# Optimization experiments

Hardware: AMD Instinct MI355X
Metric: run time of the kernel (lower is better)

## Reference

```python
import jax, jax.numpy as jnp
import numpy as np

MAX_DISP = 4  # init kwarg


def setup_inputs() -> dict:
    key = jax.random.key(0)
    k1, k2 = jax.random.split(key)
    x_1 = jax.random.normal(k1, (8, 128, 128, 128), dtype=jnp.float32)
    x_2 = jax.random.normal(k2, (8, 128, 128, 128), dtype=jnp.float32)
    return {"x_1": x_1, "x_2": x_2}


def reference(x_1, x_2):
    d = MAX_DISP
    H, W = x_1.shape[2], x_1.shape[3]
    # zero-pad x_2 by max_disp on both spatial dims (ConstantPad2d)
    x2p = jnp.pad(x_2, ((0, 0), (0, 0), (d, d), (d, d)))
    # loop over the fixed (2d+1)^2 = 81 displacement offsets (structural, not data dim)
    outs = [
        jnp.mean(x_1 * x2p[:, :, dx:dx + H, dy:dy + W], axis=1)  # [B,H,W]
        for dx in range(2 * d + 1)
        for dy in range(2 * d + 1)
    ]
    return jnp.stack(outs, axis=1)  # [B, 81, H, W]
```

## Files before the change

### kernel.cpp

```cpp
#include <hip/hip_runtime.h>


constexpr int Bn = 8, Cn = 128, Hn = 128, Wn = 128;
constexpr int HWn = Hn * Wn;
constexpr int TH = 4;
constexpr int NDH = 3;
constexpr int NR = TH + NDH - 1;
constexpr int WP = 144;
constexpr int NF4 = (NR * 140) / 4;

__global__ __launch_bounds__(256, 3)
void corr_kernel(const float* __restrict__ x1, const float* __restrict__ x2,
                 float* __restrict__ out) {
  __shared__ float s2[2][2][NR][WP];
  __shared__ float sred[128][36];

  const int t    = threadIdx.x;
  const int half = t >> 7;
  const int q    = t & 127;
  const int row  = q >> 5;
  const int w0   = (q & 31) << 2;

  const int phys = blockIdx.x;
  const int xcd  = phys & 7;
  const int slot = phys >> 3;
  const int tl   = slot / 3;
  const int g    = slot % 3;
  const int tile = xcd * 32 + tl;
  const int b    = tile >> 5;
  const int h0   = (tile & 31) * TH;
  const int dhm  = g * NDH - 4;

  const int i0 = q, i1 = q + 128;
  const int sr0 = i0 / 35, fc0 = i0 % 35;
  int sr1 = i1 / 35; const int fc1 = i1 % 35;
  const bool act1 = (i1 < NF4);
  if (sr1 > NR - 1) sr1 = NR - 1;
  const int gr0 = h0 + dhm + sr0;
  const int gr1 = h0 + dhm + sr1;
  const bool ok0 = ((unsigned)gr0 < (unsigned)Hn) && (fc0 >= 1) && (fc0 <= 32);
  const bool ok1 = act1 && ((unsigned)gr1 < (unsigned)Hn) && (fc1 >= 1) && (fc1 <= 32);
  const int off0 = gr0 * Wn + fc0 * 4 - 4;
  const int off1 = gr1 * Wn + fc1 * 4 - 4;

  const float* x1c = x1 + (size_t)b * Cn * HWn + (size_t)(half * 64) * HWn
                        + (h0 + row) * Wn + w0;
  const float* x2c = x2 + (size_t)b * Cn * HWn + (size_t)(half * 64) * HWn;

  float4 acc[NDH][9];
#pragma unroll
  for (int r = 0; r < NDH; ++r)
#pragma unroll
    for (int dw = 0; dw < 9; ++dw) acc[r][dw] = make_float4(0.f, 0.f, 0.f, 0.f);

  float4 pv0 = make_float4(0.f, 0.f, 0.f, 0.f);
  float4 pv1 = make_float4(0.f, 0.f, 0.f, 0.f);
  if (ok0) pv0 = *(const float4*)(x2c + off0);
  if (ok1) pv1 = *(const float4*)(x2c + off1);
  float4 pa = *(const float4*)x1c;

#pragma unroll 1
  for (int cc = 0; cc < 64; ++cc) {
    const int buf = cc & 1;
    *(float4*)&s2[buf][half][sr0][fc0 * 4] = pv0;
    if (act1) *(float4*)&s2[buf][half][sr1][fc1 * 4] = pv1;
    const float4 a = pa;
    if (cc < 63) {
      const float* nx2 = x2c + (size_t)(cc + 1) * HWn;
      if (ok0) pv0 = *(const float4*)(nx2 + off0);
      if (ok1) pv1 = *(const float4*)(nx2 + off1);
      pa = *(const float4*)(x1c + (size_t)(cc + 1) * HWn);
    }
    __syncthreads();

#pragma unroll
    for (int r = 0; r < NDH; ++r) {
      const float* srow = &s2[buf][half][row + r][w0];
      const float4 wa = *(const float4*)(srow);
      const float4 wb = *(const float4*)(srow + 4);
      const float4 wc = *(const float4*)(srow + 8);
      const float win[12] = {wa.x, wa.y, wa.z, wa.w, wb.x, wb.y, wb.z, wb.w,
                             wc.x, wc.y, wc.z, wc.w};
#pragma unroll
      for (int dw = 0; dw < 9; ++dw) {
        acc[r][dw].x += a.x * win[dw + 0];
        acc[r][dw].y += a.y * win[dw + 1];
        acc[r][dw].z += a.z * win[dw + 2];
        acc[r][dw].w += a.w * win[dw + 3];
      }
    }
  }

  const float scale = 1.0f / 128.0f;
  float* ob = out + (size_t)b * 81 * HWn + (size_t)(h0 + row) * Wn + w0;
#pragma unroll
  for (int r = 0; r < NDH; ++r) {
    if (half) {
#pragma unroll
      for (int dw = 0; dw < 9; ++dw) *(float4*)&sred[q][dw * 4] = acc[r][dw];
    }
    __syncthreads();
    if (!half) {
      const int obase = (g * 3 + r) * 9;
#pragma unroll
      for (int dw = 0; dw < 9; ++dw) {
        const float4 s = *(const float4*)&sred[q][dw * 4];
        const float4 m = acc[r][dw];
        float4 rz;
        rz.x = (m.x + s.x) * scale;
        rz.y = (m.y + s.y) * scale;
        rz.z = (m.z + s.z) * scale;
        rz.w = (m.w + s.w) * scale;
        *(float4*)(ob + (size_t)(obase + dw) * HWn) = rz;
      }
    }
    __syncthreads();
  }
}

extern "C" void kernel_launch(void* const* d_in, const int* in_sizes, int n_in,
                              void* d_out, int out_size, void* d_ws, size_t ws_size,
                              hipStream_t stream) {
  const float* x1 = (const float*)d_in[0];
  const float* x2 = (const float*)d_in[1];
  float* out = (float*)d_out;
  const int n_wgs = Bn * (Hn / TH) * 3;
  corr_kernel<<<dim3(n_wgs), dim3(256), 0, stream>>>(x1, x2, out);
}
```

Measured before the change: 189.1 us.

## Give each wavefront a private LDS window to drop per-channel block barriers

Splits the shared x2 staging buffer so each of the four wavefronts stages its own 4-row window for the two output rows it computes. Because each wave only reads data it wrote itself, the per-channel __syncthreads and the double buffering are removed. It relies on in-order LDS access within a single wave. The cost is some duplicated global loads of the overlapping halo rows across the two waves of each channel half, plus a third load per lane.

```diff
diff --git a/kernel.cpp b/kernel.cpp
--- a/kernel.cpp
+++ b/kernel.cpp
@@ -5,21 +5,23 @@
 constexpr int HWn = Hn * Wn;
 constexpr int TH = 4;
 constexpr int NDH = 3;
-constexpr int NR = TH + NDH - 1;
+constexpr int WR = 4;
 constexpr int WP = 144;
-constexpr int NF4 = (NR * 140) / 4;
 
 __global__ __launch_bounds__(256, 3)
 void corr_kernel(const float* __restrict__ x1, const float* __restrict__ x2,
                  float* __restrict__ out) {
-  __shared__ float s2[2][2][NR][WP];
+  __shared__ float s2[4][WR][WP];
   __shared__ float sred[128][36];
 
   const int t    = threadIdx.x;
-  const int half = t >> 7;
+  const int wv   = t >> 6;
+  const int lane = t & 63;
+  const int half = wv >> 1;
+  const int rp   = wv & 1;
   const int q    = t & 127;
-  const int row  = q >> 5;
-  const int w0   = (q & 31) << 2;
+  const int rowl = q >> 5;
+  const int w0   = (lane & 31) << 2;
 
   const int phys = blockIdx.x;
   const int xcd  = phys & 7;
@@ -31,21 +33,24 @@
   const int h0   = (tile & 31) * TH;
   const int dhm  = g * NDH - 4;
 
-  const int i0 = q, i1 = q + 128;
-  const int sr0 = i0 / 35, fc0 = i0 % 35;
-  int sr1 = i1 / 35; const int fc1 = i1 % 35;
-  const bool act1 = (i1 < NF4);
-  if (sr1 > NR - 1) sr1 = NR - 1;
-  const int gr0 = h0 + dhm + sr0;
-  const int gr1 = h0 + dhm + sr1;
-  const bool ok0 = ((unsigned)gr0 < (unsigned)Hn) && (fc0 >= 1) && (fc0 <= 32);
-  const bool ok1 = act1 && ((unsigned)gr1 < (unsigned)Hn) && (fc1 >= 1) && (fc1 <= 32);
-  const int off0 = gr0 * Wn + fc0 * 4 - 4;
-  const int off1 = gr1 * Wn + fc1 * 4 - 4;
+  const int base_row = h0 + 2 * rp + dhm;
+  const int s0i = lane, s1i = lane + 64, s2ii = lane + 128;
+  const bool act2 = (lane < 12);
+  const int sr0 = s0i / 35, fc0 = s0i % 35;
+  const int sr1 = s1i / 35, fc1 = s1i % 35;
+  const int sr2 = act2 ? s2ii / 35 : 0, fc2 = act2 ? s2ii % 35 : 0;
+  const bool ok0 = ((unsigned)(base_row + sr0) < (unsigned)Hn) && (fc0 >= 1) && (fc0 <= 32);
+  const bool ok1 = ((unsigned)(base_row + sr1) < (unsigned)Hn) && (fc1 >= 1) && (fc1 <= 32);
+  const bool ok2 = act2 && ((unsigned)(base_row + sr2) < (unsigned)Hn) && (fc2 >= 1) && (fc2 <= 32);
+  const int off0 = (base_row + sr0) * Wn + fc0 * 4 - 4;
+  const int off1 = (base_row + sr1) * Wn + fc1 * 4 - 4;
+  const int off2 = (base_row + sr2) * Wn + fc2 * 4 - 4;
+  float* lp0 = &s2[wv][sr0][fc0 * 4];
+  float* lp1 = &s2[wv][sr1][fc1 * 4];
+  float* lp2 = &s2[wv][sr2][fc2 * 4];
 
-  const float* x1c = x1 + (size_t)b * Cn * HWn + (size_t)(half * 64) * HWn
-                        + (h0 + row) * Wn + w0;
-  const float* x2c = x2 + (size_t)b * Cn * HWn + (size_t)(half * 64) * HWn;
+  const float* x1c = x1 + ((size_t)b * Cn + half * 64) * HWn + (h0 + rowl) * Wn + w0;
+  const float* x2c = x2 + ((size_t)b * Cn + half * 64) * HWn;
 
   float4 acc[NDH][9];
 #pragma unroll
@@ -55,27 +60,30 @@
 
   float4 pv0 = make_float4(0.f, 0.f, 0.f, 0.f);
   float4 pv1 = make_float4(0.f, 0.f, 0.f, 0.f);
+  float4 pv2 = make_float4(0.f, 0.f, 0.f, 0.f);
   if (ok0) pv0 = *(const float4*)(x2c + off0);
   if (ok1) pv1 = *(const float4*)(x2c + off1);
+  if (ok2) pv2 = *(const float4*)(x2c + off2);
   float4 pa = *(const float4*)x1c;
+
+  const int srow_base = lane >> 5;
 
 #pragma unroll 1
   for (int cc = 0; cc < 64; ++cc) {
-    const int buf = cc & 1;
-    *(float4*)&s2[buf][half][sr0][fc0 * 4] = pv0;
-    if (act1) *(float4*)&s2[buf][half][sr1][fc1 * 4] = pv1;
+    *(float4*)lp0 = pv0;
+    *(float4*)lp1 = pv1;
+    if (act2) *(float4*)lp2 = pv2;
     const float4 a = pa;
     if (cc < 63) {
       const float* nx2 = x2c + (size_t)(cc + 1) * HWn;
       if (ok0) pv0 = *(const float4*)(nx2 + off0);
       if (ok1) pv1 = *(const float4*)(nx2 + off1);
+      if (ok2) pv2 = *(const float4*)(nx2 + off2);
       pa = *(const float4*)(x1c + (size_t)(cc + 1) * HWn);
     }
-    __syncthreads();
-
 #pragma unroll
     for (int r = 0; r < NDH; ++r) {
-      const float* srow = &s2[buf][half][row + r][w0];
+      const float* srow = &s2[wv][srow_base + r][w0];
       const float4 wa = *(const float4*)(srow);
       const float4 wb = *(const float4*)(srow + 4);
       const float4 wc = *(const float4*)(srow + 8);
@@ -92,7 +100,7 @@
   }
 
   const float scale = 1.0f / 128.0f;
-  float* ob = out + (size_t)b * 81 * HWn + (size_t)(h0 + row) * Wn + w0;
+  float* ob = out + (size_t)b * 81 * HWn + (size_t)(h0 + rowl) * Wn + w0;
 #pragma unroll
   for (int r = 0; r < NDH; ++r) {
     if (half) {
```

Measured after the change: 191.2 us. Within noise of the previous version (+1.1%).

## Restructure correlation into single-wavefront blocks per vertical displacement without barriers

Applied to the files above, without the earlier changes.

Each workgroup becomes a single 64-lane wavefront that handles one vertical displacement over a 4-row tile. It covers all 128 channels, with each lane computing 8 pixels across the 9 horizontal displacements. This removes the channel split, the shared-memory cross-half reduction and every __syncthreads, and relies on in-order LDS access within one wavefront. In exchange, x1 and x2 tiles are re-read once per vertical displacement, 9 times instead of 3, which raises global/L2 traffic. The launch is also only 2304 single-wave blocks, which may leave each CU with few resident waves for latency hiding.

```diff
diff --git a/kernel.cpp b/kernel.cpp
--- a/kernel.cpp
+++ b/kernel.cpp
@@ -3,118 +3,105 @@
 
 constexpr int Bn = 8, Cn = 128, Hn = 128, Wn = 128;
 constexpr int HWn = Hn * Wn;
-constexpr int TH = 4;
-constexpr int NDH = 3;
-constexpr int NR = TH + NDH - 1;
-constexpr int WP = 144;
-constexpr int NF4 = (NR * 140) / 4;
+constexpr int ROWF = 136;
+constexpr int NSLOT = 4 * 34;
 
-__global__ __launch_bounds__(256, 3)
+__global__ __launch_bounds__(64, 3)
 void corr_kernel(const float* __restrict__ x1, const float* __restrict__ x2,
                  float* __restrict__ out) {
-  __shared__ float s2[2][2][NR][WP];
-  __shared__ float sred[128][36];
+  __shared__ float s2[4 * ROWF];
 
-  const int t    = threadIdx.x;
-  const int half = t >> 7;
-  const int q    = t & 127;
-  const int row  = q >> 5;
-  const int w0   = (q & 31) << 2;
+  const int lane = threadIdx.x;
+  const int rl   = lane >> 4;
+  const int px0  = (lane & 15) << 3;
 
   const int phys = blockIdx.x;
-  const int xcd  = phys & 7;
+  const int b    = phys & 7;
   const int slot = phys >> 3;
-  const int tl   = slot / 3;
-  const int g    = slot % 3;
-  const int tile = xcd * 32 + tl;
-  const int b    = tile >> 5;
-  const int h0   = (tile & 31) * TH;
-  const int dhm  = g * NDH - 4;
+  const int dh   = slot % 9 - 4;
+  const int h0   = (slot / 9) * 4;
 
-  const int i0 = q, i1 = q + 128;
-  const int sr0 = i0 / 35, fc0 = i0 % 35;
-  int sr1 = i1 / 35; const int fc1 = i1 % 35;
-  const bool act1 = (i1 < NF4);
-  if (sr1 > NR - 1) sr1 = NR - 1;
-  const int gr0 = h0 + dhm + sr0;
-  const int gr1 = h0 + dhm + sr1;
+  const int s0i = lane, s1i = lane + 64, s2i = lane + 128;
+  const bool act2 = (lane < NSLOT - 128);
+  const int sr0 = s0i / 34, fc0 = s0i % 34;
+  const int sr1 = s1i / 34, fc1 = s1i % 34;
+  const int sr2 = act2 ? s2i / 34 : 0, fc2 = act2 ? s2i % 34 : 0;
+  const int gr0 = h0 + sr0 + dh, gr1 = h0 + sr1 + dh, gr2 = h0 + sr2 + dh;
   const bool ok0 = ((unsigned)gr0 < (unsigned)Hn) && (fc0 >= 1) && (fc0 <= 32);
-  const bool ok1 = act1 && ((unsigned)gr1 < (unsigned)Hn) && (fc1 >= 1) && (fc1 <= 32);
+  const bool ok1 = ((unsigned)gr1 < (unsigned)Hn) && (fc1 >= 1) && (fc1 <= 32);
+  const bool ok2 = act2 && ((unsigned)gr2 < (unsigned)Hn) && (fc2 >= 1) && (fc2 <= 32);
   const int off0 = gr0 * Wn + fc0 * 4 - 4;
   const int off1 = gr1 * Wn + fc1 * 4 - 4;
+  const int off2 = gr2 * Wn + fc2 * 4 - 4;
+  float* lp0 = &s2[sr0 * ROWF + fc0 * 4];
+  float* lp1 = &s2[sr1 * ROWF + fc1 * 4];
+  float* lp2 = &s2[sr2 * ROWF + fc2 * 4];
+  const float* srow = &s2[rl * ROWF + px0];
 
-  const float* x1c = x1 + (size_t)b * Cn * HWn + (size_t)(half * 64) * HWn
-                        + (h0 + row) * Wn + w0;
-  const float* x2c = x2 + (size_t)b * Cn * HWn + (size_t)(half * 64) * HWn;
+  const float* x1c = x1 + (size_t)b * Cn * HWn + (h0 + rl) * Wn + px0;
+  const float* x2c = x2 + (size_t)b * Cn * HWn;
 
-  float4 acc[NDH][9];
+  float4 acc[9][2];
 #pragma unroll
-  for (int r = 0; r < NDH; ++r)
-#pragma unroll
-    for (int dw = 0; dw < 9; ++dw) acc[r][dw] = make_float4(0.f, 0.f, 0.f, 0.f);
+  for (int dw = 0; dw < 9; ++dw) {
+    acc[dw][0] = make_float4(0.f, 0.f, 0.f, 0.f);
+    acc[dw][1] = make_float4(0.f, 0.f, 0.f, 0.f);
+  }
 
   float4 pv0 = make_float4(0.f, 0.f, 0.f, 0.f);
   float4 pv1 = make_float4(0.f, 0.f, 0.f, 0.f);
+  float4 pv2 = make_float4(0.f, 0.f, 0.f, 0.f);
   if (ok0) pv0 = *(const float4*)(x2c + off0);
   if (ok1) pv1 = *(const float4*)(x2c + off1);
-  float4 pa = *(const float4*)x1c;
+  if (ok2) pv2 = *(const float4*)(x2c + off2);
+  float4 pa0 = *(const float4*)(x1c);
+  float4 pa1 = *(const float4*)(x1c + 4);
 
 #pragma unroll 1
-  for (int cc = 0; cc < 64; ++cc) {
-    const int buf = cc & 1;
-    *(float4*)&s2[buf][half][sr0][fc0 * 4] = pv0;
-    if (act1) *(float4*)&s2[buf][half][sr1][fc1 * 4] = pv1;
-    const float4 a = pa;
-    if (cc < 63) {
+  for (int cc = 0; cc < 128; ++cc) {
+    *(float4*)lp0 = pv0;
+    *(float4*)lp1 = pv1;
+    if (act2) *(float4*)lp2 = pv2;
+    const float4 a0 = pa0, a1 = pa1;
+    if (cc < 127) {
       const float* nx2 = x2c + (size_t)(cc + 1) * HWn;
       if (ok0) pv0 = *(const float4*)(nx2 + off0);
       if (ok1) pv1 = *(const float4*)(nx2 + off1);
-      pa = *(const float4*)(x1c + (size_t)(cc + 1) * HWn);
+      if (ok2) pv2 = *(const float4*)(nx2 + off2);
+      const float* nx1 = x1c + (size_t)(cc + 1) * HWn;
+      pa0 = *(const float4*)(nx1);
+      pa1 = *(const float4*)(nx1 + 4);
     }
-    __syncthreads();
-
+    const float4 w0 = *(const float4*)(srow);
+    const float4 w1 = *(const float4*)(srow + 4);
+    const float4 w2 = *(const float4*)(srow + 8);
+    const float4 w3 = *(const float4*)(srow + 12);
+    const float win[16] = {w0.x, w0.y, w0.z, w0.w, w1.x, w1.y, w1.z, w1.w,
+                           w2.x, w2.y, w2.z, w2.w, w3.x, w3.y, w3.z, w3.w};
+    const float av[8] = {a0.x, a0.y, a0.z, a0.w, a1.x, a1.y, a1.z, a1.w};
 #pragma unroll
-    for (int r = 0; r < NDH; ++r) {
-      const float* srow = &s2[buf][half][row + r][w0];
-      const float4 wa = *(const float4*)(srow);
-      const float4 wb = *(const float4*)(srow + 4);
-      const float4 wc = *(const float4*)(srow + 8);
-      const float win[12] = {wa.x, wa.y, wa.z, wa.w, wb.x, wb.y, wb.z, wb.w,
-                             wc.x, wc.y, wc.z, wc.w};
-#pragma unroll
-      for (int dw = 0; dw < 9; ++dw) {
-        acc[r][dw].x += a.x * win[dw + 0];
-        acc[r][dw].y += a.y * win[dw + 1];
-        acc[r][dw].z += a.z * win[dw + 2];
-        acc[r][dw].w += a.w * win[dw + 3];
-      }
+    for (int dw = 0; dw < 9; ++dw) {
+      acc[dw][0].x += av[0] * win[dw + 0];
+      acc[dw][0].y += av[1] * win[dw + 1];
+      acc[dw][0].z += av[2] * win[dw + 2];
+      acc[dw][0].w += av[3] * win[dw + 3];
+      acc[dw][1].x += av[4] * win[dw + 4];
+      acc[dw][1].y += av[5] * win[dw + 5];
+      acc[dw][1].z += av[6] * win[dw + 6];
+      acc[dw][1].w += av[7] * win[dw + 7];
     }
   }
 
   const float scale = 1.0f / 128.0f;
-  float* ob = out + (size_t)b * 81 * HWn + (size_t)(h0 + row) * Wn + w0;
+  const int obase = (dh + 4) * 9;
+  float* ob = out + ((size_t)b * 81 + obase) * HWn + (size_t)(h0 + rl) * Wn + px0;
 #pragma unroll
-  for (int r = 0; r < NDH; ++r) {
-    if (half) {
-#pragma unroll
-      for (int dw = 0; dw < 9; ++dw) *(float4*)&sred[q][dw * 4] = acc[r][dw];
-    }
-    __syncthreads();
-    if (!half) {
-      const int obase = (g * 3 + r) * 9;
-#pragma unroll
-      for (int dw = 0; dw < 9; ++dw) {
-        const float4 s = *(const float4*)&sred[q][dw * 4];
-        const float4 m = acc[r][dw];
-        float4 rz;
-        rz.x = (m.x + s.x) * scale;
-        rz.y = (m.y + s.y) * scale;
-        rz.z = (m.z + s.z) * scale;
-        rz.w = (m.w + s.w) * scale;
-        *(float4*)(ob + (size_t)(obase + dw) * HWn) = rz;
-      }
-    }
-    __syncthreads();
+  for (int dw = 0; dw < 9; ++dw) {
+    float4 lo = acc[dw][0], hi = acc[dw][1];
+    lo.x *= scale; lo.y *= scale; lo.z *= scale; lo.w *= scale;
+    hi.x *= scale; hi.y *= scale; hi.z *= scale; hi.w *= scale;
+    *(float4*)(ob + (size_t)dw * HWn)     = lo;
+    *(float4*)(ob + (size_t)dw * HWn + 4) = hi;
   }
 }
 
@@ -124,6 +111,6 @@
   const float* x1 = (const float*)d_in[0];
   const float* x2 = (const float*)d_in[1];
   float* out = (float*)d_out;
-  const int n_wgs = Bn * (Hn / TH) * 3;
-  corr_kernel<<<dim3(n_wgs), dim3(256), 0, stream>>>(x1, x2, out);
+  const int n_wgs = Bn * 9 * (Hn / 4);
+  corr_kernel<<<dim3(n_wgs), dim3(64), 0, stream>>>(x1, x2, out);
 }
```

After: 240.7 us. +27.3%, slower.
